# Optimization experiments

Measured on AMD Instinct MI355X. Metric: run time of the kernel, lower is better.

The kernel has to match this reference:

```python
import jax, jax.numpy as jnp
import numpy as np

N_NODES = 100000
N_EDGES = 1600000


def setup_inputs() -> dict:
    key = jax.random.key(0)
    ks = jax.random.split(key, 6)
    x = jax.random.normal(ks[0], (N_NODES, 128), dtype=jnp.float32)
    edge_index = jax.random.randint(ks[1], (2, N_EDGES), 0, N_NODES, dtype=jnp.int64)
    # glorot-ish scaled weights
    W0 = jax.random.normal(ks[2], (128, 64), dtype=jnp.float32) * (1.0 / np.sqrt(128))
    W1 = jax.random.normal(ks[3], (64, 64), dtype=jnp.float32) * (1.0 / np.sqrt(64))
    W2 = jax.random.normal(ks[4], (64, 40), dtype=jnp.float32) * (1.0 / np.sqrt(64))
    b0 = jnp.zeros((64,), jnp.float32)
    b1 = jnp.zeros((64,), jnp.float32)
    b2 = jnp.zeros((40,), jnp.float32)
    return {"x": x, "edge_index": edge_index, "W0": W0, "b0": b0,
            "W1": W1, "b1": b1, "W2": W2, "b2": b2}


def _gcn_norm(edge_index, n, dtype):
    # PyG gcn_norm: add self-loops, deg over targets, norm = d^-1/2[src]*d^-1/2[dst]
    loop = jnp.arange(n, dtype=edge_index.dtype)
    src = jnp.concatenate([edge_index[0], loop])
    dst = jnp.concatenate([edge_index[1], loop])
    deg = jax.ops.segment_sum(jnp.ones_like(dst, dtype=dtype), dst, num_segments=n)
    dinv = jnp.where(deg > 0, jax.lax.rsqrt(deg), 0.0)
    return src, dst, dinv[src] * dinv[dst]


def reference(x, edge_index, W0, b0, W1, b1, W2, b2):
    n = x.shape[0]
    src, dst, norm = _gcn_norm(edge_index, n, x.dtype)

    def conv(h, W, b):
        h = h @ W                                   # [N, out]
        msg = h[src] * norm[:, None]                # gather + per-edge scale
        return jax.ops.segment_sum(msg, dst, num_segments=n) + b

    # dropout skipped (eval mode); relu between layers per forward()
    h = jax.nn.relu(conv(x, W0, b0))
    h = jax.nn.relu(conv(h, W1, b1))
    return conv(h, W2, b2)
```

## Files before the change

kernel.cpp:

```cpp
#include <hip/hip_runtime.h>
#include <hip/hip_fp16.h>


#define ALIGN256(x) (((size_t)(x) + 255) & ~(size_t)255)

typedef _Float16 f16;
typedef f16 f16x8 __attribute__((ext_vector_type(8)));
typedef float f32x4 __attribute__((ext_vector_type(4)));


__global__ __launch_bounds__(256) void k_coarse(const int* __restrict__ ei,
                                                int* __restrict__ ccnt,
                                                int E, int NBUK) {
    __shared__ int h[512];
    int t = threadIdx.x;
    for (int i = t; i < NBUK; i += 256) h[i] = 0;
    __syncthreads();
    int e0 = blockIdx.x * 8192;
    int e1 = min(e0 + 8192, E);
    for (int e = e0 + t; e < e1; e += 256) atomicAdd(&h[ei[E + e] >> 8], 1);
    __syncthreads();
    for (int i = t; i < NBUK; i += 256) {
        int c = h[i];
        if (c) atomicAdd(&ccnt[i], c);
    }
}


__global__ __launch_bounds__(256) void k_cscan(const int* __restrict__ ccnt,
                                               int* __restrict__ cbase,
                                               int* __restrict__ cpos,
                                               int* __restrict__ row_start,
                                               int NBUK, int E, int N) {
    __shared__ int sd[256];
    int t = threadIdx.x;
    int i0 = 2 * t, i1 = 2 * t + 1;
    int v0 = (i0 < NBUK) ? ccnt[i0] : 0;
    int v1 = (i1 < NBUK) ? ccnt[i1] : 0;
    int s = v0 + v1;
    sd[t] = s;
    __syncthreads();
    for (int off = 1; off < 256; off <<= 1) {
        int u = (t >= off) ? sd[t - off] : 0;
        __syncthreads();
        sd[t] += u;
        __syncthreads();
    }
    int base = sd[t] - s;
    if (i0 < NBUK) { cbase[i0] = base;      cpos[i0] = base; }
    if (i1 < NBUK) { cbase[i1] = base + v0; cpos[i1] = base + v0; }
    if (t == 0) { cbase[NBUK] = E; row_start[N] = E; }
}


__global__ __launch_bounds__(256) void k_passA(const int* __restrict__ ei,
                                               int* __restrict__ cpos,
                                               unsigned int* __restrict__ stage,
                                               int E, int NBUK) {
    __shared__ int h[512];
    __shared__ int base[512];
    int t = threadIdx.x;
    for (int i = t; i < NBUK; i += 256) h[i] = 0;
    __syncthreads();
    int e0 = blockIdx.x * 8192;
    int e1 = min(e0 + 8192, E);
    for (int e = e0 + t; e < e1; e += 256) atomicAdd(&h[ei[E + e] >> 8], 1);
    __syncthreads();
    for (int b = t; b < NBUK; b += 256) {
        int c = h[b];
        base[b] = c ? atomicAdd(&cpos[b], c) : 0;
        h[b] = 0;
    }
    __syncthreads();
    for (int e = e0 + t; e < e1; e += 256) {
        unsigned int s = (unsigned int)ei[e];
        int d = ei[E + e];
        int b = d >> 8;
        int off = base[b] + atomicAdd(&h[b], 1);
        stage[off] = ((unsigned int)(d & 255) << 24) | s;
    }
}


__global__ __launch_bounds__(256) void k_B1(const unsigned int* __restrict__ stage,
                                            const int* __restrict__ cbase,
                                            int* __restrict__ row_start,
                                            float* __restrict__ dinv, int N) {
    __shared__ int cnt[256];
    __shared__ int sd[256];
    int b = blockIdx.x;
    int n0 = b << 8;
    int t = threadIdx.x;
    cnt[t] = 0;
    __syncthreads();
    int s0 = cbase[b], s1 = cbase[b + 1];
    for (int j = s0 + t; j < s1; j += 256) atomicAdd(&cnt[stage[j] >> 24], 1);
    __syncthreads();
    int c = cnt[t];
    sd[t] = c;
    __syncthreads();
    for (int off = 1; off < 256; off <<= 1) {
        int u = (t >= off) ? sd[t - off] : 0;
        __syncthreads();
        sd[t] += u;
        __syncthreads();
    }
    int excl = sd[t] - c;
    int node = n0 + t;
    if (node < N) {
        row_start[node] = s0 + excl;
        dinv[node] = 1.0f / sqrtf((float)(c + 1));
    }
}


__global__ __launch_bounds__(256) void k_B2(const unsigned int* __restrict__ stage,
                                            const int* __restrict__ cbase,
                                            const int* __restrict__ row_start,
                                            const float* __restrict__ dinv,
                                            int2* __restrict__ ep, int N) {
    __shared__ int lpos[256];
    __shared__ float ld[256];
    int b = blockIdx.x;
    int n0 = b << 8;
    int t = threadIdx.x;
    int node = n0 + t;
    if (node < N) {
        lpos[t] = row_start[node];
        ld[t] = dinv[node];
    }
    __syncthreads();
    int s0 = cbase[b], s1 = cbase[b + 1];
    for (int j = s0 + t; j < s1; j += 256) {
        unsigned int v = stage[j];
        int li = v >> 24;
        int src = v & 0xFFFFFF;
        int slot = atomicAdd(&lpos[li], 1);
        ep[slot] = make_int2(src, __float_as_int(dinv[src] * ld[li]));
    }
}


template <int K, int OUT, int NF, typename XT>
__global__ __launch_bounds__(256) void k_mgemm(const XT* __restrict__ X,
                                               const float* __restrict__ W,
                                               __half* __restrict__ Y, int N) {
    constexpr int NC = NF * 16;
    constexpr int NT = K / 32;
    __shared__ f16 Wl[NT * NF * 4 * 128];

    int tid = threadIdx.x;
    for (int idx = tid; idx < K * NC; idx += 256) {
        int k = idx / NC;
        int n = idx - k * NC;
        float v = (n < OUT) ? W[k * OUT + n] : 0.0f;
        int t = k >> 5, h = (k >> 3) & 3, j = k & 7, f = n >> 4, nn = n & 15;
        Wl[((t * NF + f) * 4 + h) * 128 + nn * 8 + j] = (f16)v;
    }
    __syncthreads();

    int lane = tid & 63;
    int wid = tid >> 6;
    int h = lane >> 4;
    int nn = lane & 15;
    int row = blockIdx.x * 64 + (wid << 4) + nn;
    bool valid = row < N;

    f32x4 acc[NF];
#pragma unroll
    for (int f = 0; f < NF; ++f) acc[f] = (f32x4){0.f, 0.f, 0.f, 0.f};

#pragma unroll
    for (int t = 0; t < NT; ++t) {
        f16x8 xf;
        if (valid) {
            if constexpr (sizeof(XT) == 4) {
                const float* xp = (const float*)X + (size_t)row * K + (t << 5) + (h << 3);
                float4 u0 = *(const float4*)xp;
                float4 u1 = *(const float4*)(xp + 4);
                xf[0] = (f16)u0.x; xf[1] = (f16)u0.y; xf[2] = (f16)u0.z; xf[3] = (f16)u0.w;
                xf[4] = (f16)u1.x; xf[5] = (f16)u1.y; xf[6] = (f16)u1.z; xf[7] = (f16)u1.w;
            } else {
                xf = *(const f16x8*)((const __half*)X + (size_t)row * K + (t << 5) + (h << 3));
            }
        } else {
#pragma unroll
            for (int j = 0; j < 8; ++j) xf[j] = (f16)0.f;
        }
#pragma unroll
        for (int f = 0; f < NF; ++f) {
            f16x8 wf = *(const f16x8*)&Wl[((t * NF + f) * 4 + h) * 128 + nn * 8];
            acc[f] = __builtin_amdgcn_mfma_f32_16x16x32_f16(wf, xf, acc[f], 0, 0, 0);
        }
    }

    if (valid) {
#pragma unroll
        for (int f = 0; f < NF; ++f) {
            int c = (f << 4) + (h << 2);
            if (c < OUT) {
                __half2 p0 = __floats2half2_rn(acc[f][0], acc[f][1]);
                __half2 p1 = __floats2half2_rn(acc[f][2], acc[f][3]);
                uint2 pk = make_uint2(*(unsigned int*)&p0, *(unsigned int*)&p1);
                *(uint2*)&Y[(size_t)row * OUT + c] = pk;
            }
        }
    }
}


__device__ __forceinline__ void fma8(float4& a0, float4& a1, uint4 hv, float w) {
    __half2* hp = (__half2*)&hv;
    float2 f0 = __half22float2(hp[0]);
    float2 f1 = __half22float2(hp[1]);
    float2 f2 = __half22float2(hp[2]);
    float2 f3 = __half22float2(hp[3]);
    a0.x += f0.x * w; a0.y += f0.y * w; a0.z += f1.x * w; a0.w += f1.y * w;
    a1.x += f2.x * w; a1.y += f2.y * w; a1.z += f3.x * w; a1.w += f3.y * w;
}

template <int NV, int F, int RELU, typename OutT>
__global__ __launch_bounds__(256) void k_agg(const __half* __restrict__ H,
                                             const int* __restrict__ row_start,
                                             const int2* __restrict__ ep,
                                             const float* __restrict__ dinv,
                                             const float* __restrict__ bias,
                                             OutT* __restrict__ out, int N) {
    int tid = threadIdx.x;
    int lane = tid & 63;
    int sub = lane >> 3;
    int lq = lane & 7;
    int node = blockIdx.x * 32 + (tid >> 6) * 8 + sub;
    if (node >= N) return;
    const bool act = (NV == 8) || (lq < NV);

    int jb = row_start[node];
    int je = row_start[node + 1];
    float dv = dinv[node];

    float4 a0 = make_float4(0.f, 0.f, 0.f, 0.f);
    float4 a1 = make_float4(0.f, 0.f, 0.f, 0.f);
    if (act) {
        uint4 hv = *(const uint4*)&H[(size_t)node * F + 8 * lq];
        fma8(a0, a1, hv, dv * dv);
    }

    int j = jb;
    for (; j + 8 <= je; j += 8) {
        int2 e0 = ep[j],     e1 = ep[j + 1], e2 = ep[j + 2], e3 = ep[j + 3];
        int2 e4 = ep[j + 4], e5 = ep[j + 5], e6 = ep[j + 6], e7 = ep[j + 7];
        if (act) {
            uint4 h0 = *(const uint4*)&H[(size_t)e0.x * F + 8 * lq];
            uint4 h1 = *(const uint4*)&H[(size_t)e1.x * F + 8 * lq];
            uint4 h2 = *(const uint4*)&H[(size_t)e2.x * F + 8 * lq];
            uint4 h3 = *(const uint4*)&H[(size_t)e3.x * F + 8 * lq];
            uint4 h4 = *(const uint4*)&H[(size_t)e4.x * F + 8 * lq];
            uint4 h5 = *(const uint4*)&H[(size_t)e5.x * F + 8 * lq];
            uint4 h6 = *(const uint4*)&H[(size_t)e6.x * F + 8 * lq];
            uint4 h7 = *(const uint4*)&H[(size_t)e7.x * F + 8 * lq];
            fma8(a0, a1, h0, __int_as_float(e0.y));
            fma8(a0, a1, h1, __int_as_float(e1.y));
            fma8(a0, a1, h2, __int_as_float(e2.y));
            fma8(a0, a1, h3, __int_as_float(e3.y));
            fma8(a0, a1, h4, __int_as_float(e4.y));
            fma8(a0, a1, h5, __int_as_float(e5.y));
            fma8(a0, a1, h6, __int_as_float(e6.y));
            fma8(a0, a1, h7, __int_as_float(e7.y));
        }
    }
    for (; j + 2 <= je; j += 2) {
        int2 e0 = ep[j], e1 = ep[j + 1];
        if (act) {
            uint4 h0 = *(const uint4*)&H[(size_t)e0.x * F + 8 * lq];
            uint4 h1 = *(const uint4*)&H[(size_t)e1.x * F + 8 * lq];
            fma8(a0, a1, h0, __int_as_float(e0.y));
            fma8(a0, a1, h1, __int_as_float(e1.y));
        }
    }
    if (j < je) {
        int2 e = ep[j];
        if (act) {
            uint4 h = *(const uint4*)&H[(size_t)e.x * F + 8 * lq];
            fma8(a0, a1, h, __int_as_float(e.y));
        }
    }

    if (act) {
        float4 b0 = *(const float4*)&bias[8 * lq];
        float4 b1 = *(const float4*)&bias[8 * lq + 4];
        a0.x += b0.x; a0.y += b0.y; a0.z += b0.z; a0.w += b0.w;
        a1.x += b1.x; a1.y += b1.y; a1.z += b1.z; a1.w += b1.w;
        if (RELU) {
            a0.x = fmaxf(a0.x, 0.f); a0.y = fmaxf(a0.y, 0.f);
            a0.z = fmaxf(a0.z, 0.f); a0.w = fmaxf(a0.w, 0.f);
            a1.x = fmaxf(a1.x, 0.f); a1.y = fmaxf(a1.y, 0.f);
            a1.z = fmaxf(a1.z, 0.f); a1.w = fmaxf(a1.w, 0.f);
        }
        if constexpr (sizeof(OutT) == 2) {
            __half2 p0 = __floats2half2_rn(a0.x, a0.y);
            __half2 p1 = __floats2half2_rn(a0.z, a0.w);
            __half2 p2 = __floats2half2_rn(a1.x, a1.y);
            __half2 p3 = __floats2half2_rn(a1.z, a1.w);
            uint4 pk = make_uint4(*(unsigned int*)&p0, *(unsigned int*)&p1,
                                  *(unsigned int*)&p2, *(unsigned int*)&p3);
            *(uint4*)&out[(size_t)node * F + 8 * lq] = pk;
        } else {
            *(float4*)&out[(size_t)node * F + 8 * lq] = a0;
            *(float4*)&out[(size_t)node * F + 8 * lq + 4] = a1;
        }
    }
}


extern "C" void kernel_launch(void* const* d_in, const int* in_sizes, int n_in,
                              void* d_out, int out_size, void* d_ws, size_t ws_size,
                              hipStream_t stream) {
    const float* x  = (const float*)d_in[0];
    const int*   ei = (const int*)d_in[1];
    const float* W0 = (const float*)d_in[2];
    const float* b0 = (const float*)d_in[3];
    const float* W1 = (const float*)d_in[4];
    const float* b1 = (const float*)d_in[5];
    const float* W2 = (const float*)d_in[6];
    const float* b2 = (const float*)d_in[7];
    float* out = (float*)d_out;

    const int N = in_sizes[0] / 128;
    const int E = in_sizes[1] / 2;
    const int NBUK = (N + 255) >> 8;

    char* w = (char*)d_ws;
    size_t off = 0;
    int*    ccnt      = (int*)(w + off);    off = ALIGN256(off + (size_t)NBUK * 4);
    int*    cbase     = (int*)(w + off);    off = ALIGN256(off + (size_t)(NBUK + 1) * 4);
    int*    cpos      = (int*)(w + off);    off = ALIGN256(off + (size_t)NBUK * 4);
    int*    row_start = (int*)(w + off);    off = ALIGN256(off + (size_t)(N + 1) * 4);
    float*  dinv      = (float*)(w + off);  off = ALIGN256(off + (size_t)N * 4);
    int2*   ep        = (int2*)(w + off);   off = ALIGN256(off + (size_t)E * 8);
    __half* bufH      = (__half*)(w + off); off = ALIGN256(off + (size_t)N * 64 * 2);
    __half* bufG      = (__half*)(w + off); off = ALIGN256(off + (size_t)N * 64 * 2);
    unsigned int* stage = (unsigned int*)bufG;

    const int gGemm = (N + 63) / 64;
    const int gAgg  = (N + 31) / 32;
    const int gPA   = (E + 8191) / 8192;

    hipMemsetAsync(ccnt, 0, (size_t)NBUK * 4, stream);
    k_mgemm<128, 64, 4><<<gGemm, 256, 0, stream>>>(x, W0, bufH, N);
    k_coarse<<<gPA, 256, 0, stream>>>(ei, ccnt, E, NBUK);
    k_cscan<<<1, 256, 0, stream>>>(ccnt, cbase, cpos, row_start, NBUK, E, N);
    k_passA<<<gPA, 256, 0, stream>>>(ei, cpos, stage, E, NBUK);
    k_B1<<<NBUK, 256, 0, stream>>>(stage, cbase, row_start, dinv, N);
    k_B2<<<NBUK, 256, 0, stream>>>(stage, cbase, row_start, dinv, ep, N);

    k_agg<8, 64, 1, __half><<<gAgg, 256, 0, stream>>>(bufH, row_start, ep, dinv, b0, bufG, N);
    k_mgemm<64, 64, 4><<<gGemm, 256, 0, stream>>>(bufG, W1, bufH, N);
    k_agg<8, 64, 1, __half><<<gAgg, 256, 0, stream>>>(bufH, row_start, ep, dinv, b1, bufG, N);
    k_mgemm<64, 40, 3><<<gGemm, 256, 0, stream>>>(bufG, W2, bufH, N);
    k_agg<5, 40, 0, float><<<gAgg, 256, 0, stream>>>(bufH, row_start, ep, dinv, b2, out, N);
}
```

Measured before the change: 304.8 us.

## Fuse bucket scan into coarse histogram via last-block, add nontemporal loads, shrink agg unroll

Result: slower. 334.8 us (+9.8%).

```diff
diff --git a/kernel.cpp b/kernel.cpp
--- a/kernel.cpp
+++ b/kernel.cpp
@@ -11,8 +11,13 @@
 
 __global__ __launch_bounds__(256) void k_coarse(const int* __restrict__ ei,
                                                 int* __restrict__ ccnt,
-                                                int E, int NBUK) {
+                                                int* __restrict__ done,
+                                                int* __restrict__ cbase,
+                                                int* __restrict__ cpos,
+                                                int* __restrict__ row_start,
+                                                int E, int N, int NBUK, int nblk) {
     __shared__ int h[512];
+    __shared__ int lastblk;
     int t = threadIdx.x;
     for (int i = t; i < NBUK; i += 256) h[i] = 0;
     __syncthreads();
@@ -24,16 +29,12 @@
         int c = h[i];
         if (c) atomicAdd(&ccnt[i], c);
     }
-}
-
-
-__global__ __launch_bounds__(256) void k_cscan(const int* __restrict__ ccnt,
-                                               int* __restrict__ cbase,
-                                               int* __restrict__ cpos,
-                                               int* __restrict__ row_start,
-                                               int NBUK, int E, int N) {
+    __threadfence();
+    if (t == 0) lastblk = (atomicAdd(done, 1) == nblk - 1) ? 1 : 0;
+    __syncthreads();
+    if (!lastblk) return;
+
     __shared__ int sd[256];
-    int t = threadIdx.x;
     int i0 = 2 * t, i1 = 2 * t + 1;
     int v0 = (i0 < NBUK) ? ccnt[i0] : 0;
     int v1 = (i1 < NBUK) ? ccnt[i1] : 0;
@@ -73,8 +74,8 @@
     }
     __syncthreads();
     for (int e = e0 + t; e < e1; e += 256) {
-        unsigned int s = (unsigned int)ei[e];
-        int d = ei[E + e];
+        unsigned int s = (unsigned int)__builtin_nontemporal_load(&ei[e]);
+        int d = __builtin_nontemporal_load(&ei[E + e]);
         int b = d >> 8;
         int off = base[b] + atomicAdd(&h[b], 1);
         stage[off] = ((unsigned int)(d & 255) << 24) | s;
@@ -132,7 +133,7 @@
     __syncthreads();
     int s0 = cbase[b], s1 = cbase[b + 1];
     for (int j = s0 + t; j < s1; j += 256) {
-        unsigned int v = stage[j];
+        unsigned int v = __builtin_nontemporal_load(&stage[j]);
         int li = v >> 24;
         int src = v & 0xFFFFFF;
         int slot = atomicAdd(&lpos[li], 1);
@@ -220,12 +221,12 @@
 }
 
 template <int NV, int F, int RELU, typename OutT>
-__global__ __launch_bounds__(256) void k_agg(const __half* __restrict__ H,
-                                             const int* __restrict__ row_start,
-                                             const int2* __restrict__ ep,
-                                             const float* __restrict__ dinv,
-                                             const float* __restrict__ bias,
-                                             OutT* __restrict__ out, int N) {
+__global__ __launch_bounds__(256, 8) void k_agg(const __half* __restrict__ H,
+                                                const int* __restrict__ row_start,
+                                                const int2* __restrict__ ep,
+                                                const float* __restrict__ dinv,
+                                                const float* __restrict__ bias,
+                                                OutT* __restrict__ out, int N) {
     int tid = threadIdx.x;
     int lane = tid & 63;
     int sub = lane >> 3;
@@ -245,43 +246,31 @@
         fma8(a0, a1, hv, dv * dv);
     }
 
+    const unsigned long long* epq = (const unsigned long long*)ep;
     int j = jb;
-    for (; j + 8 <= je; j += 8) {
-        int2 e0 = ep[j],     e1 = ep[j + 1], e2 = ep[j + 2], e3 = ep[j + 3];
-        int2 e4 = ep[j + 4], e5 = ep[j + 5], e6 = ep[j + 6], e7 = ep[j + 7];
+    for (; j + 4 <= je; j += 4) {
+        unsigned long long u0 = __builtin_nontemporal_load(&epq[j]);
+        unsigned long long u1 = __builtin_nontemporal_load(&epq[j + 1]);
+        unsigned long long u2 = __builtin_nontemporal_load(&epq[j + 2]);
+        unsigned long long u3 = __builtin_nontemporal_load(&epq[j + 3]);
         if (act) {
-            uint4 h0 = *(const uint4*)&H[(size_t)e0.x * F + 8 * lq];
-            uint4 h1 = *(const uint4*)&H[(size_t)e1.x * F + 8 * lq];
-            uint4 h2 = *(const uint4*)&H[(size_t)e2.x * F + 8 * lq];
-            uint4 h3 = *(const uint4*)&H[(size_t)e3.x * F + 8 * lq];
-            uint4 h4 = *(const uint4*)&H[(size_t)e4.x * F + 8 * lq];
-            uint4 h5 = *(const uint4*)&H[(size_t)e5.x * F + 8 * lq];
-            uint4 h6 = *(const uint4*)&H[(size_t)e6.x * F + 8 * lq];
-            uint4 h7 = *(const uint4*)&H[(size_t)e7.x * F + 8 * lq];
-            fma8(a0, a1, h0, __int_as_float(e0.y));
-            fma8(a0, a1, h1, __int_as_float(e1.y));
-            fma8(a0, a1, h2, __int_as_float(e2.y));
-            fma8(a0, a1, h3, __int_as_float(e3.y));
-            fma8(a0, a1, h4, __int_as_float(e4.y));
-            fma8(a0, a1, h5, __int_as_float(e5.y));
-            fma8(a0, a1, h6, __int_as_float(e6.y));
-            fma8(a0, a1, h7, __int_as_float(e7.y));
-        }
-    }
-    for (; j + 2 <= je; j += 2) {
-        int2 e0 = ep[j], e1 = ep[j + 1];
+            int s0 = (int)(u0 & 0xffffffffu), s1 = (int)(u1 & 0xffffffffu);
+            int s2 = (int)(u2 & 0xffffffffu), s3 = (int)(u3 & 0xffffffffu);
+            uint4 h0 = *(const uint4*)&H[(size_t)s0 * F + 8 * lq];
+            uint4 h1 = *(const uint4*)&H[(size_t)s1 * F + 8 * lq];
+            uint4 h2 = *(const uint4*)&H[(size_t)s2 * F + 8 * lq];
+            uint4 h3 = *(const uint4*)&H[(size_t)s3 * F + 8 * lq];
+            fma8(a0, a1, h0, __uint_as_float((unsigned)(u0 >> 32)));
+            fma8(a0, a1, h1, __uint_as_float((unsigned)(u1 >> 32)));
+            fma8(a0, a1, h2, __uint_as_float((unsigned)(u2 >> 32)));
+            fma8(a0, a1, h3, __uint_as_float((unsigned)(u3 >> 32)));
+        }
+    }
+    for (; j < je; ++j) {
+        unsigned long long u = __builtin_nontemporal_load(&epq[j]);
         if (act) {
-            uint4 h0 = *(const uint4*)&H[(size_t)e0.x * F + 8 * lq];
-            uint4 h1 = *(const uint4*)&H[(size_t)e1.x * F + 8 * lq];
-            fma8(a0, a1, h0, __int_as_float(e0.y));
-            fma8(a0, a1, h1, __int_as_float(e1.y));
-        }
-    }
-    if (j < je) {
-        int2 e = ep[j];
-        if (act) {
-            uint4 h = *(const uint4*)&H[(size_t)e.x * F + 8 * lq];
-            fma8(a0, a1, h, __int_as_float(e.y));
+            uint4 h = *(const uint4*)&H[(size_t)(int)(u & 0xffffffffu) * F + 8 * lq];
+            fma8(a0, a1, h, __uint_as_float((unsigned)(u >> 32)));
         }
     }
 
@@ -331,7 +320,8 @@
 
     char* w = (char*)d_ws;
     size_t off = 0;
-    int*    ccnt      = (int*)(w + off);    off = ALIGN256(off + (size_t)NBUK * 4);
+    int*    ccnt      = (int*)(w + off);    off = ALIGN256(off + (size_t)(NBUK + 1) * 4);
+    int*    done      = ccnt + NBUK;
     int*    cbase     = (int*)(w + off);    off = ALIGN256(off + (size_t)(NBUK + 1) * 4);
     int*    cpos      = (int*)(w + off);    off = ALIGN256(off + (size_t)NBUK * 4);
     int*    row_start = (int*)(w + off);    off = ALIGN256(off + (size_t)(N + 1) * 4);
@@ -345,10 +335,9 @@
     const int gAgg  = (N + 31) / 32;
     const int gPA   = (E + 8191) / 8192;
 
-    hipMemsetAsync(ccnt, 0, (size_t)NBUK * 4, stream);
+    hipMemsetAsync(ccnt, 0, (size_t)(NBUK + 1) * 4, stream);
     k_mgemm<128, 64, 4><<<gGemm, 256, 0, stream>>>(x, W0, bufH, N);
-    k_coarse<<<gPA, 256, 0, stream>>>(ei, ccnt, E, NBUK);
-    k_cscan<<<1, 256, 0, stream>>>(ccnt, cbase, cpos, row_start, NBUK, E, N);
+    k_coarse<<<gPA, 256, 0, stream>>>(ei, ccnt, done, cbase, cpos, row_start, E, N, NBUK, gPA);
     k_passA<<<gPA, 256, 0, stream>>>(ei, cpos, stage, E, NBUK);
     k_B1<<<NBUK, 256, 0, stream>>>(stage, cbase, row_start, dinv, N);
     k_B2<<<NBUK, 256, 0, stream>>>(stage, cbase, row_start, dinv, ep, N);
```
